# Kernel optimization log

Hardware: AMD Instinct MI355X
Metric: run time of the kernel (lower is better)

Reference implementation:

```python
import jax, jax.numpy as jnp
import numpy as np

EPS = 1e-6

def l2norm(x):
    return x / jnp.maximum(jnp.linalg.norm(x, axis=-1, keepdims=True), 1e-12)

def setup_inputs() -> dict:
    key = jax.random.key(0)
    ks = jax.random.split(key, 16)
    B, V, L = 64, 197, 64
    Dv, Dt, E = 768, 768, 256
    s = (2.0 / E) ** 0.5  # kaiming fan_out scale
    inp = {
        'visual_cls': jax.random.normal(ks[0], (B, Dv), jnp.float32),
        'textual_cls': jax.random.normal(ks[1], (B, Dt), jnp.float32),
        'visual_tokens': jax.random.normal(ks[2], (B, V, Dv), jnp.float32),
        'textual_tokens': jax.random.normal(ks[3], (B, L, Dt), jnp.float32),
        'text_length': jnp.maximum(jax.random.randint(ks[4], (B,), 0, L, jnp.int32), 1),
        'Wv': jax.random.normal(ks[5], (Dv, E), jnp.float32) * s,
        'bv': jnp.zeros((E,), jnp.float32),
        'Wt': jax.random.normal(ks[6], (Dt, E), jnp.float32) * s,
        'bt': jnp.zeros((E,), jnp.float32),
        'Wvt': jax.random.normal(ks[7], (Dv, E), jnp.float32) * s,
        'bvt': jnp.zeros((E,), jnp.float32),
        'Wtt': jax.random.normal(ks[8], (Dt, E), jnp.float32) * s,
        'btt': jnp.zeros((E,), jnp.float32),
    }
    return inp

def reference(visual_cls, textual_cls, visual_tokens, textual_tokens, text_length,
              Wv, bv, Wt, bt, Wvt, bvt, Wtt, btt):
    # cls projections
    v_cls = visual_cls @ Wv + bv            # [B, E]
    t_cls = textual_cls @ Wt + bt           # [B, E]
    # token projections + l2 normalize
    v_tok = l2norm(visual_tokens @ Wvt + bvt)   # [B, V, E]
    t_tok = l2norm(textual_tokens @ Wtt + btt)  # [B, L, E]
    B, V, E = v_tok.shape
    L = t_tok.shape[1]
    # full cross-modal token similarity (this is the kernel target)
    sim = jnp.einsum('bvd,qtd->bqvt', v_tok, t_tok)  # [B, Q, V, T]
    # image->text: max over text tokens, plain mean over visual tokens
    image_to_text = jnp.max(sim, axis=-1)            # [B, Q, V]
    image_to_text_sim = jnp.sum(image_to_text, axis=-1) / V  # [B, Q]
    # text->image: max over visual tokens, masked mean over text tokens
    text_to_image = jnp.max(sim, axis=-2)            # [B, Q, T]
    # faithful to original: mask indexed by FIRST batch axis b
    mask = jnp.arange(L)[None, :] >= text_length[:, None]   # [B, T]
    mask3 = mask[:, None, :]                                 # [B, 1, T]
    numer = jnp.sum(jnp.where(mask3, 0.0, text_to_image), axis=-1)
    denom = jnp.maximum(jnp.sum(~mask3, axis=-1).astype(text_to_image.dtype), EPS)
    text_to_image_sim = numer / denom                # [B, Q]
    return (v_cls, t_cls, image_to_text_sim, text_to_image_sim)
```

## Files before the change

### kernel.cpp

```cpp
#include <hip/hip_runtime.h>
#include <hip/hip_bf16.h>

#define NB 64
#define NV 197
#define NL 64
#define ND 768
#define NE 256

typedef __attribute__((ext_vector_type(8))) short bh8;
typedef __attribute__((ext_vector_type(16))) float f32x16;

__device__ inline ushort f2bf(float x) {
  __hip_bfloat16 h = __float2bfloat16(x);
  return *reinterpret_cast<ushort*>(&h);
}

__device__ inline bh8 cvt8(float4 a, float4 b) {
  union { bh8 v; ushort u[8]; } r;
  r.u[0] = f2bf(a.x); r.u[1] = f2bf(a.y); r.u[2] = f2bf(a.z); r.u[3] = f2bf(a.w);
  r.u[4] = f2bf(b.x); r.u[5] = f2bf(b.y); r.u[6] = f2bf(b.z); r.u[7] = f2bf(b.w);
  return r.v;
}

__global__ __launch_bounds__(256) void wcvt_kernel(
    const float* __restrict__ W0, const float* __restrict__ W1,
    const float* __restrict__ W2, const float* __restrict__ W3,
    ushort* __restrict__ O0, ushort* __restrict__ O1,
    ushort* __restrict__ O2, ushort* __restrict__ O3) {
  const float* Win; ushort* Wout;
  switch (blockIdx.y) {
    case 0: Win = W0; Wout = O0; break;
    case 1: Win = W1; Wout = O1; break;
    case 2: Win = W2; Wout = O2; break;
    default: Win = W3; Wout = O3; break;
  }
  const int ks = blockIdx.x;
  const int t = threadIdx.x;
  const int l = t & 63;
  const int lr = l & 31, hi = l >> 5;
  const int kbase = ks * 16 + hi * 8;
#pragma unroll
  for (int i = 0; i < 2; ++i) {
    const int nt = (t >> 6) + i * 4;
    const int n = nt * 32 + lr;
    union { bh8 v; ushort u[8]; } f;
#pragma unroll
    for (int e = 0; e < 8; ++e)
      f.u[e] = f2bf(Win[(size_t)(kbase + e) * NE + n]);
    *(bh8*)&Wout[(size_t)((nt * 48 + ks) * 64 + l) * 8] = f.v;
  }
}

__device__ inline int aswz(int row, int cbyte) {
  return ((row * 256 + cbyte) ^ ((row & 15) << 4)) >> 2;
}

__global__ __launch_bounds__(256, 2) void proj_kernel(
    const float* __restrict__ Xv, const float* __restrict__ Xt,
    const float* __restrict__ Xcv, const float* __restrict__ Xct,
    const ushort* __restrict__ Fv, const ushort* __restrict__ Ft,
    const ushort* __restrict__ Fcv, const ushort* __restrict__ Fct,
    const float* __restrict__ bvt, const float* __restrict__ btt,
    const float* __restrict__ bv, const float* __restrict__ bt,
    ushort* __restrict__ v_tok, ushort* __restrict__ t_tok,
    float* __restrict__ v_cls, float* __restrict__ t_cls) {
  __shared__ float a_lds[64 * 64];
  __shared__ float ssq_lds[2][2][32];

  const int blk = blockIdx.x;
  const float* X; const ushort* F; const float* bias;
  ushort* outb = nullptr; float* outf = nullptr;
  int row0; bool norm;
  if (blk < 197)       { X = Xv;  F = Fv;  bias = bvt; outb = v_tok; row0 = blk * 64;         norm = true; }
  else if (blk < 261)  { X = Xt;  F = Ft;  bias = btt; outb = t_tok; row0 = (blk - 197) * 64; norm = true; }
  else if (blk == 261) { X = Xcv; F = Fcv; bias = bv;  outf = v_cls; row0 = 0;                norm = false; }
  else                 { X = Xct; F = Fct; bias = bt;  outf = t_cls; row0 = 0;                norm = false; }

  const int t = threadIdx.x;
  const int l = t & 63, w = t >> 6;
  const int lr = l & 31, hi = l >> 5;
  const int wr = w & 1, wc = w >> 1;

  const int srow = t >> 2;
  const int scq = t & 3;
  const float* Xrow = X + (size_t)(row0 + srow) * ND;

  const int arow = wr * 32 + lr;
  const ushort* Fw = F + ((size_t)(wc * 4 * 48) * 64 + l) * 8;

  f32x16 acc0 = {0}, acc1 = {0}, acc2 = {0}, acc3 = {0};

  float4 g0, g1, g2, g3, n0, n1, n2, n3;
#define GLOAD(d0, d1, d2, d3, kc) \
  d0 = *(const float4*)(Xrow + (kc) + scq * 4); \
  d1 = *(const float4*)(Xrow + (kc) + 16 + scq * 4); \
  d2 = *(const float4*)(Xrow + (kc) + 32 + scq * 4); \
  d3 = *(const float4*)(Xrow + (kc) + 48 + scq * 4);

  GLOAD(g0, g1, g2, g3, 0)
  for (int c = 0; c < 12; ++c) {
    if (c) __syncthreads();
    *(float4*)&a_lds[aswz(srow, scq * 16)]       = g0;
    *(float4*)&a_lds[aswz(srow, 64 + scq * 16)]  = g1;
    *(float4*)&a_lds[aswz(srow, 128 + scq * 16)] = g2;
    *(float4*)&a_lds[aswz(srow, 192 + scq * 16)] = g3;
    if (c < 11) { GLOAD(n0, n1, n2, n3, (c + 1) * 64) }
    __syncthreads();

#pragma unroll
    for (int ksl = 0; ksl < 4; ++ksl) {
      const int ks = c * 4 + ksl;
      float4 af0 = *(const float4*)&a_lds[aswz(arow, ksl * 64 + hi * 32)];
      float4 af1 = *(const float4*)&a_lds[aswz(arow, ksl * 64 + hi * 32 + 16)];
      bh8 b0 = *(const bh8*)(Fw + (size_t)(0 * 48 + ks) * 64 * 8);
      bh8 b1 = *(const bh8*)(Fw + (size_t)(1 * 48 + ks) * 64 * 8);
      bh8 b2 = *(const bh8*)(Fw + (size_t)(2 * 48 + ks) * 64 * 8);
      bh8 b3 = *(const bh8*)(Fw + (size_t)(3 * 48 + ks) * 64 * 8);
      bh8 af = cvt8(af0, af1);
      acc0 = __builtin_amdgcn_mfma_f32_32x32x16_bf16(af, b0, acc0, 0, 0, 0);
      acc1 = __builtin_amdgcn_mfma_f32_32x32x16_bf16(af, b1, acc1, 0, 0, 0);
      acc2 = __builtin_amdgcn_mfma_f32_32x32x16_bf16(af, b2, acc2, 0, 0, 0);
      acc3 = __builtin_amdgcn_mfma_f32_32x32x16_bf16(af, b3, acc3, 0, 0, 0);
    }
    g0 = n0; g1 = n1; g2 = n2; g3 = n3;
  }
#undef GLOAD

  const float bn0 = bias[wc * 128 + lr];
  const float bn1 = bias[wc * 128 + 32 + lr];
  const float bn2 = bias[wc * 128 + 64 + lr];
  const float bn3 = bias[wc * 128 + 96 + lr];
#pragma unroll
  for (int r = 0; r < 16; ++r) {
    acc0[r] += bn0; acc1[r] += bn1; acc2[r] += bn2; acc3[r] += bn3;
  }

  if (norm) {
    float p[16];
#pragma unroll
    for (int r = 0; r < 16; ++r)
      p[r] = acc0[r] * acc0[r] + acc1[r] * acc1[r] +
             acc2[r] * acc2[r] + acc3[r] * acc3[r];
#pragma unroll
    for (int off = 1; off < 32; off <<= 1) {
#pragma unroll
      for (int r = 0; r < 16; ++r) p[r] += __shfl_xor(p[r], off);
    }
    if (lr == 0) {
#pragma unroll
      for (int r = 0; r < 16; ++r)
        ssq_lds[wc][wr][(r & 3) + 8 * (r >> 2) + 4 * hi] = p[r];
    }
    __syncthreads();
#pragma unroll
    for (int r = 0; r < 16; ++r) {
      const int R = (r & 3) + 8 * (r >> 2) + 4 * hi;
      const float s = ssq_lds[0][wr][R] + ssq_lds[1][wr][R];
      const float scale = 1.0f / fmaxf(sqrtf(s), 1e-12f);
      ushort* orow = outb + (size_t)(row0 + wr * 32 + R) * NE + wc * 128 + lr;
      orow[0]  = f2bf(acc0[r] * scale);
      orow[32] = f2bf(acc1[r] * scale);
      orow[64] = f2bf(acc2[r] * scale);
      orow[96] = f2bf(acc3[r] * scale);
    }
  } else {
#pragma unroll
    for (int r = 0; r < 16; ++r) {
      const int R = (r & 3) + 8 * (r >> 2) + 4 * hi;
      float* orow = outf + (size_t)(row0 + wr * 32 + R) * NE + wc * 128 + lr;
      orow[0]  = acc0[r];
      orow[32] = acc1[r];
      orow[64] = acc2[r];
      orow[96] = acc3[r];
    }
  }
}

__global__ __launch_bounds__(256, 2) void sim_kernel(
    const __hip_bfloat16* __restrict__ vt,
    const __hip_bfloat16* __restrict__ tt,
    const int* __restrict__ tlen,
    float* __restrict__ out_i2t,
    float* __restrict__ out_t2i) {
  __shared__ float red[4][4][64];
  __shared__ float wsum[4][4];

  const int blk = blockIdx.x;
  const int q = blk & 63;
  const int bc = blk >> 6;
  const int tid = threadIdx.x;
  const int l = tid & 63;
  const int w = tid >> 6;
  const int lr = l & 31;
  const int hi = l >> 5;
  const size_t bstride = (size_t)NV * NE;

  bh8 breg0[16], breg1[16];
  {
    const __hip_bfloat16* T0 = tt + ((size_t)(q * NL) + lr) * NE + hi * 8;
    const __hip_bfloat16* T1 = T0 + 32 * NE;
#pragma unroll
    for (int s = 0; s < 16; ++s) {
      breg0[s] = *(const bh8*)(T0 + s * 16);
      breg1[s] = *(const bh8*)(T1 + s * 16);
    }
  }

  const int r0 = 32 * w + lr;
  const int r1 = min(128 + 32 * w + lr, NV - 1);

  const __hip_bfloat16* A0 = vt + (size_t)(bc * 4) * bstride + (size_t)r0 * NE + hi * 8;
  const __hip_bfloat16* A1 = vt + (size_t)(bc * 4) * bstride + (size_t)r1 * NE + hi * 8;

  bh8 a0[4], a1[4];
#pragma unroll
  for (int s = 0; s < 4; ++s) {
    a0[s] = *(const bh8*)(A0 + s * 16);
    a1[s] = *(const bh8*)(A1 + s * 16);
  }

  for (int ib = 0; ib < 4; ++ib) {
    f32x16 acc00 = {0}, acc01 = {0}, acc10 = {0}, acc11 = {0};

    __builtin_amdgcn_s_setprio(1);
#pragma unroll
    for (int s = 0; s < 16; ++s) {
      bh8 va0 = a0[s & 3], va1 = a1[s & 3];
      const int sn = s + 4;
      const size_t off = (size_t)(sn & 15) * 16 + (size_t)(sn >> 4) * bstride;
      a0[s & 3] = *(const bh8*)(A0 + off);
      a1[s & 3] = *(const bh8*)(A1 + off);
      acc00 = __builtin_amdgcn_mfma_f32_32x32x16_bf16(va0, breg0[s], acc00, 0, 0, 0);
      acc01 = __builtin_amdgcn_mfma_f32_32x32x16_bf16(va0, breg1[s], acc01, 0, 0, 0);
      acc10 = __builtin_amdgcn_mfma_f32_32x32x16_bf16(va1, breg0[s], acc10, 0, 0, 0);
      acc11 = __builtin_amdgcn_mfma_f32_32x32x16_bf16(va1, breg1[s], acc11, 0, 0, 0);
    }
    __builtin_amdgcn_s_setprio(0);
    A0 += bstride;
    A1 += bstride;

    float i2t_sum = 0.0f;
#pragma unroll
    for (int r = 0; r < 16; ++r) {
      {
        float m = fmaxf(acc00[r], acc01[r]);
        m = fmaxf(m, __shfl_xor(m, 1));
        m = fmaxf(m, __shfl_xor(m, 2));
        m = fmaxf(m, __shfl_xor(m, 4));
        m = fmaxf(m, __shfl_xor(m, 8));
        m = fmaxf(m, __shfl_xor(m, 16));
        i2t_sum += m;
      }
      {
        float m = fmaxf(acc10[r], acc11[r]);
        m = fmaxf(m, __shfl_xor(m, 1));
        m = fmaxf(m, __shfl_xor(m, 2));
        m = fmaxf(m, __shfl_xor(m, 4));
        m = fmaxf(m, __shfl_xor(m, 8));
        m = fmaxf(m, __shfl_xor(m, 16));
        const int row = 128 + 32 * w + (r & 3) + 8 * (r >> 2) + 4 * hi;
        if (row < NV) i2t_sum += m;
      }
    }
    i2t_sum += __shfl_xor(i2t_sum, 32);
    if (l == 0) wsum[ib][w] = i2t_sum;

    float vm0 = -1e30f, vm1 = -1e30f;
#pragma unroll
    for (int r = 0; r < 16; ++r) {
      vm0 = fmaxf(vm0, fmaxf(acc00[r], acc10[r]));
      vm1 = fmaxf(vm1, fmaxf(acc01[r], acc11[r]));
    }
    vm0 = fmaxf(vm0, __shfl_xor(vm0, 32));
    vm1 = fmaxf(vm1, __shfl_xor(vm1, 32));
    if (hi == 0) red[ib][w][lr] = vm0;
    else         red[ib][w][32 + lr] = vm1;
  }

  __syncthreads();

  {
    const int ib = w;
    const int b = bc * 4 + ib;
    const int len = tlen[b];
    float m = fmaxf(fmaxf(red[ib][0][l], red[ib][1][l]),
                    fmaxf(red[ib][2][l], red[ib][3][l]));
    float v = (l < len) ? m : 0.0f;
#pragma unroll
    for (int off = 1; off < 64; off <<= 1) v += __shfl_xor(v, off);
    if (l == 0) {
      out_t2i[b * NB + q] = v / fmaxf((float)len, 1e-6f);
      out_i2t[b * NB + q] = (wsum[ib][0] + wsum[ib][1] +
                             wsum[ib][2] + wsum[ib][3]) / (float)NV;
    }
  }
}

extern "C" void kernel_launch(void* const* d_in, const int* in_sizes, int n_in,
                              void* d_out, int out_size, void* d_ws, size_t ws_size,
                              hipStream_t stream) {
  (void)in_sizes; (void)n_in; (void)out_size; (void)ws_size;
  const float* visual_cls    = (const float*)d_in[0];
  const float* textual_cls   = (const float*)d_in[1];
  const float* visual_tokens = (const float*)d_in[2];
  const float* textual_tokens= (const float*)d_in[3];
  const int*   text_length   = (const int*)d_in[4];
  const float* Wv  = (const float*)d_in[5];
  const float* bv  = (const float*)d_in[6];
  const float* Wt  = (const float*)d_in[7];
  const float* bt  = (const float*)d_in[8];
  const float* Wvt = (const float*)d_in[9];
  const float* bvt = (const float*)d_in[10];
  const float* Wtt = (const float*)d_in[11];
  const float* btt = (const float*)d_in[12];

  float* out   = (float*)d_out;
  float* v_cls = out;
  float* t_cls = out + NB * NE;
  float* i2t   = out + 2 * NB * NE;
  float* t2i   = i2t + NB * NB;

  ushort* wsb   = (ushort*)d_ws;
  ushort* v_tok = wsb;
  ushort* t_tok = v_tok + (size_t)NB * NV * NE;
  ushort* Fv    = t_tok + (size_t)NB * NL * NE;
  ushort* Ft    = Fv + (size_t)8 * 48 * 64 * 8;
  ushort* Fcv   = Ft + (size_t)8 * 48 * 64 * 8;
  ushort* Fct   = Fcv + (size_t)8 * 48 * 64 * 8;

  wcvt_kernel<<<dim3(48, 4), 256, 0, stream>>>(Wvt, Wtt, Wv, Wt,
                                               Fv, Ft, Fcv, Fct);
  proj_kernel<<<263, 256, 0, stream>>>(visual_tokens, textual_tokens,
                                       visual_cls, textual_cls,
                                       Fv, Ft, Fcv, Fct,
                                       bvt, btt, bv, bt,
                                       v_tok, t_tok, v_cls, t_cls);
  sim_kernel<<<NB * NB / 4, 256, 0, stream>>>((const __hip_bfloat16*)v_tok,
                                              (const __hip_bfloat16*)t_tok,
                                              text_length, i2t, t2i);
}
```

Measured before the change: 234.2 us.

## Store text tokens in MFMA fragment layout and stage them through LDS in sim kernel

The projection kernel now writes normalized text tokens directly in the MFMA operand fragment order, so the similarity kernel can bulk-copy one query's 64x256 text block into LDS instead of holding 32 fragments in registers. Each wave now handles one batch image and walks all visual-token tiles, keeping running column maxima in registers rather than reducing through shared memory across four batches per wave. Occupancy hint rises to 3 blocks per SM because register pressure drops. The cost is an extra 32 KB LDS fill per block and per-k LDS reads that replace register-resident operands.

```diff
diff --git a/kernel.cpp b/kernel.cpp
--- a/kernel.cpp
+++ b/kernel.cpp
@@ -51,10 +51,6 @@
   }
 }
 
-__device__ inline int aswz(int row, int cbyte) {
-  return ((row * 256 + cbyte) ^ ((row & 15) << 4)) >> 2;
-}
-
 __global__ __launch_bounds__(256, 2) void proj_kernel(
     const float* __restrict__ Xv, const float* __restrict__ Xt,
     const float* __restrict__ Xcv, const float* __restrict__ Xct,
@@ -62,7 +58,7 @@
     const ushort* __restrict__ Fcv, const ushort* __restrict__ Fct,
     const float* __restrict__ bvt, const float* __restrict__ btt,
     const float* __restrict__ bv, const float* __restrict__ bt,
-    ushort* __restrict__ v_tok, ushort* __restrict__ t_tok,
+    ushort* __restrict__ v_tok, ushort* __restrict__ t_frag,
     float* __restrict__ v_cls, float* __restrict__ t_cls) {
   __shared__ float a_lds[64 * 64];
   __shared__ float ssq_lds[2][2][32];
@@ -70,11 +66,11 @@
   const int blk = blockIdx.x;
   const float* X; const ushort* F; const float* bias;
   ushort* outb = nullptr; float* outf = nullptr;
-  int row0; bool norm;
-  if (blk < 197)       { X = Xv;  F = Fv;  bias = bvt; outb = v_tok; row0 = blk * 64;         norm = true; }
-  else if (blk < 261)  { X = Xt;  F = Ft;  bias = btt; outb = t_tok; row0 = (blk - 197) * 64; norm = true; }
-  else if (blk == 261) { X = Xcv; F = Fcv; bias = bv;  outf = v_cls; row0 = 0;                norm = false; }
-  else                 { X = Xct; F = Fct; bias = bt;  outf = t_cls; row0 = 0;                norm = false; }
+  int row0; bool norm; bool tfrag = false;
+  if (blk < 197)       { X = Xv;  F = Fv;  bias = bvt; outb = v_tok;  row0 = blk * 64;         norm = true; }
+  else if (blk < 261)  { X = Xt;  F = Ft;  bias = btt; outb = t_frag; row0 = (blk - 197) * 64; norm = true; tfrag = true; }
+  else if (blk == 261) { X = Xcv; F = Fcv; bias = bv;  outf = v_cls;  row0 = 0;                norm = false; }
+  else                 { X = Xct; F = Fct; bias = bt;  outf = t_cls;  row0 = 0;                norm = false; }
 
   const int t = threadIdx.x;
   const int l = t & 63, w = t >> 6;
@@ -97,21 +93,23 @@
   d2 = *(const float4*)(Xrow + (kc) + 32 + scq * 4); \
   d3 = *(const float4*)(Xrow + (kc) + 48 + scq * 4);
 
+#define ASWZ(row, cbyte) ((((row) * 256 + (cbyte)) ^ (((row) & 15) << 4)) >> 2)
+
   GLOAD(g0, g1, g2, g3, 0)
   for (int c = 0; c < 12; ++c) {
     if (c) __syncthreads();
-    *(float4*)&a_lds[aswz(srow, scq * 16)]       = g0;
-    *(float4*)&a_lds[aswz(srow, 64 + scq * 16)]  = g1;
-    *(float4*)&a_lds[aswz(srow, 128 + scq * 16)] = g2;
-    *(float4*)&a_lds[aswz(srow, 192 + scq * 16)] = g3;
+    *(float4*)&a_lds[ASWZ(srow, scq * 16)]       = g0;
+    *(float4*)&a_lds[ASWZ(srow, 64 + scq * 16)]  = g1;
+    *(float4*)&a_lds[ASWZ(srow, 128 + scq * 16)] = g2;
+    *(float4*)&a_lds[ASWZ(srow, 192 + scq * 16)] = g3;
     if (c < 11) { GLOAD(n0, n1, n2, n3, (c + 1) * 64) }
     __syncthreads();
 
 #pragma unroll
     for (int ksl = 0; ksl < 4; ++ksl) {
       const int ks = c * 4 + ksl;
-      float4 af0 = *(const float4*)&a_lds[aswz(arow, ksl * 64 + hi * 32)];
-      float4 af1 = *(const float4*)&a_lds[aswz(arow, ksl * 64 + hi * 32 + 16)];
+      float4 af0 = *(const float4*)&a_lds[ASWZ(arow, ksl * 64 + hi * 32)];
+      float4 af1 = *(const float4*)&a_lds[ASWZ(arow, ksl * 64 + hi * 32 + 16)];
       bh8 b0 = *(const bh8*)(Fw + (size_t)(0 * 48 + ks) * 64 * 8);
       bh8 b1 = *(const bh8*)(Fw + (size_t)(1 * 48 + ks) * 64 * 8);
       bh8 b2 = *(const bh8*)(Fw + (size_t)(2 * 48 + ks) * 64 * 8);
@@ -125,6 +123,7 @@
     g0 = n0; g1 = n1; g2 = n2; g3 = n3;
   }
 #undef GLOAD
+#undef ASWZ
 
   const float bn0 = bias[wc * 128 + lr];
   const float bn1 = bias[wc * 128 + 32 + lr];
@@ -152,16 +151,34 @@
         ssq_lds[wc][wr][(r & 3) + 8 * (r >> 2) + 4 * hi] = p[r];
     }
     __syncthreads();
-#pragma unroll
-    for (int r = 0; r < 16; ++r) {
-      const int R = (r & 3) + 8 * (r >> 2) + 4 * hi;
-      const float s = ssq_lds[0][wr][R] + ssq_lds[1][wr][R];
-      const float scale = 1.0f / fmaxf(sqrtf(s), 1e-12f);
-      ushort* orow = outb + (size_t)(row0 + wr * 32 + R) * NE + wc * 128 + lr;
-      orow[0]  = f2bf(acc0[r] * scale);
-      orow[32] = f2bf(acc1[r] * scale);
-      orow[64] = f2bf(acc2[r] * scale);
-      orow[96] = f2bf(acc3[r] * scale);
+    if (!tfrag) {
+#pragma unroll
+      for (int r = 0; r < 16; ++r) {
+        const int R = (r & 3) + 8 * (r >> 2) + 4 * hi;
+        const float s = ssq_lds[0][wr][R] + ssq_lds[1][wr][R];
+        const float scale = 1.0f / fmaxf(sqrtf(s), 1e-12f);
+        ushort* orow = outb + (size_t)(row0 + wr * 32 + R) * NE + wc * 128 + lr;
+        orow[0]  = f2bf(acc0[r] * scale);
+        orow[32] = f2bf(acc1[r] * scale);
+        orow[64] = f2bf(acc2[r] * scale);
+        orow[96] = f2bf(acc3[r] * scale);
+      }
+    } else {
+      ushort* tq = outb + (size_t)(row0 >> 6) * 16384;
+      const int cA = lr >> 4;
+      const int cB = ((lr >> 3) & 1) * 32;
+      const int cE = lr & 7;
+#pragma unroll
+      for (int r = 0; r < 16; ++r) {
+        const int R = (r & 3) + 8 * (r >> 2) + 4 * hi;
+        const float s = ssq_lds[0][wr][R] + ssq_lds[1][wr][R];
+        const float scale = 1.0f / fmaxf(sqrtf(s), 1e-12f);
+        const int base = ((wr * 16 + wc * 8 + cA) * 64 + R + cB) * 8 + cE;
+        tq[base]        = f2bf(acc0[r] * scale);
+        tq[base + 1024] = f2bf(acc1[r] * scale);
+        tq[base + 2048] = f2bf(acc2[r] * scale);
+        tq[base + 3072] = f2bf(acc3[r] * scale);
+      }
     }
   } else {
 #pragma unroll
@@ -176,123 +193,112 @@
   }
 }
 
-__global__ __launch_bounds__(256, 2) void sim_kernel(
-    const __hip_bfloat16* __restrict__ vt,
-    const __hip_bfloat16* __restrict__ tt,
+__global__ __launch_bounds__(256, 3) void sim_kernel(
+    const ushort* __restrict__ vt, const ushort* __restrict__ tfrag,
     const int* __restrict__ tlen,
-    float* __restrict__ out_i2t,
-    float* __restrict__ out_t2i) {
-  __shared__ float red[4][4][64];
-  __shared__ float wsum[4][4];
+    float* __restrict__ out_i2t, float* __restrict__ out_t2i) {
+  __shared__ ushort t_lds[16384];
 
   const int blk = blockIdx.x;
   const int q = blk & 63;
   const int bc = blk >> 6;
   const int tid = threadIdx.x;
-  const int l = tid & 63;
-  const int w = tid >> 6;
-  const int lr = l & 31;
-  const int hi = l >> 5;
-  const size_t bstride = (size_t)NV * NE;
-
-  bh8 breg0[16], breg1[16];
+
   {
-    const __hip_bfloat16* T0 = tt + ((size_t)(q * NL) + lr) * NE + hi * 8;
-    const __hip_bfloat16* T1 = T0 + 32 * NE;
-#pragma unroll
-    for (int s = 0; s < 16; ++s) {
-      breg0[s] = *(const bh8*)(T0 + s * 16);
-      breg1[s] = *(const bh8*)(T1 + s * 16);
-    }
-  }
-
-  const int r0 = 32 * w + lr;
-  const int r1 = min(128 + 32 * w + lr, NV - 1);
-
-  const __hip_bfloat16* A0 = vt + (size_t)(bc * 4) * bstride + (size_t)r0 * NE + hi * 8;
-  const __hip_bfloat16* A1 = vt + (size_t)(bc * 4) * bstride + (size_t)r1 * NE + hi * 8;
-
-  bh8 a0[4], a1[4];
+    const bh8* src = (const bh8*)(tfrag + (size_t)q * 16384);
+    bh8* dst = (bh8*)t_lds;
+#pragma unroll
+    for (int j = 0; j < 8; ++j) dst[tid + j * 256] = src[tid + j * 256];
+  }
+  __syncthreads();
+
+  const int l = tid & 63, w = tid >> 6;
+  const int lr = l & 31, hi = l >> 5;
+  const int b = bc * 4 + w;
+  const int len = tlen[b];
+  const ushort* Vb = vt + (size_t)b * NV * NE + hi * 8;
+
+  int offA[4], offB[4];
+#pragma unroll
+  for (int p = 0; p < 4; ++p) {
+    offA[p] = min(p * 64 + lr, NV - 1) * NE;
+    offB[p] = min(p * 64 + 32 + lr, NV - 1) * NE;
+  }
+
+  bh8 rA[4], rB[4];
 #pragma unroll
   for (int s = 0; s < 4; ++s) {
-    a0[s] = *(const bh8*)(A0 + s * 16);
-    a1[s] = *(const bh8*)(A1 + s * 16);
-  }
-
-  for (int ib = 0; ib < 4; ++ib) {
-    f32x16 acc00 = {0}, acc01 = {0}, acc10 = {0}, acc11 = {0};
-
+    rA[s] = *(const bh8*)(Vb + offA[0] + s * 16);
+    rB[s] = *(const bh8*)(Vb + offB[0] + s * 16);
+  }
+
+  f32x16 vmax0, vmax1;
+#pragma unroll
+  for (int r = 0; r < 16; ++r) { vmax0[r] = -1e30f; vmax1[r] = -1e30f; }
+  float i2t_sum = 0.0f;
+
+#pragma unroll
+  for (int p = 0; p < 4; ++p) {
+    f32x16 a00 = {0}, a01 = {0}, a10 = {0}, a11 = {0};
     __builtin_amdgcn_s_setprio(1);
 #pragma unroll
-    for (int s = 0; s < 16; ++s) {
-      bh8 va0 = a0[s & 3], va1 = a1[s & 3];
-      const int sn = s + 4;
-      const size_t off = (size_t)(sn & 15) * 16 + (size_t)(sn >> 4) * bstride;
-      a0[s & 3] = *(const bh8*)(A0 + off);
-      a1[s & 3] = *(const bh8*)(A1 + off);
-      acc00 = __builtin_amdgcn_mfma_f32_32x32x16_bf16(va0, breg0[s], acc00, 0, 0, 0);
-      acc01 = __builtin_amdgcn_mfma_f32_32x32x16_bf16(va0, breg1[s], acc01, 0, 0, 0);
-      acc10 = __builtin_amdgcn_mfma_f32_32x32x16_bf16(va1, breg0[s], acc10, 0, 0, 0);
-      acc11 = __builtin_amdgcn_mfma_f32_32x32x16_bf16(va1, breg1[s], acc11, 0, 0, 0);
+    for (int ks = 0; ks < 16; ++ks) {
+      bh8 ta0 = *(const bh8*)&t_lds[(size_t)(ks * 64 + l) * 8];
+      bh8 ta1 = *(const bh8*)&t_lds[(size_t)((16 + ks) * 64 + l) * 8];
+      bh8 vb0 = rA[ks & 3], vb1 = rB[ks & 3];
+      int sn = p * 16 + ks + 4; if (sn > 63) sn = 63;
+      const int p2 = sn >> 4, k2 = sn & 15;
+      rA[ks & 3] = *(const bh8*)(Vb + offA[p2] + k2 * 16);
+      rB[ks & 3] = *(const bh8*)(Vb + offB[p2] + k2 * 16);
+      a00 = __builtin_amdgcn_mfma_f32_32x32x16_bf16(ta0, vb0, a00, 0, 0, 0);
+      a01 = __builtin_amdgcn_mfma_f32_32x32x16_bf16(ta0, vb1, a01, 0, 0, 0);
+      a10 = __builtin_amdgcn_mfma_f32_32x32x16_bf16(ta1, vb0, a10, 0, 0, 0);
+      a11 = __builtin_amdgcn_mfma_f32_32x32x16_bf16(ta1, vb1, a11, 0, 0, 0);
     }
     __builtin_amdgcn_s_setprio(0);
-    A0 += bstride;
-    A1 += bstride;
-
-    float i2t_sum = 0.0f;
+
+    {
+      float m0 = fmaxf(a00[0], a10[0]);
+#pragma unroll
+      for (int r = 1; r < 16; ++r) m0 = fmaxf(m0, fmaxf(a00[r], a10[r]));
+      m0 = fmaxf(m0, __shfl_xor(m0, 32));
+      if ((p * 64 + lr) < NV && hi == 0) i2t_sum += m0;
+      float m1 = fmaxf(a01[0], a11[0]);
+#pragma unroll
+      for (int r = 1; r < 16; ++r) m1 = fmaxf(m1, fmaxf(a01[r], a11[r]));
+      m1 = fmaxf(m1, __shfl_xor(m1, 32));
+      if ((p * 64 + 32 + lr) < NV && hi == 0) i2t_sum += m1;
+    }
 #pragma unroll
     for (int r = 0; r < 16; ++r) {
-      {
-        float m = fmaxf(acc00[r], acc01[r]);
-        m = fmaxf(m, __shfl_xor(m, 1));
-        m = fmaxf(m, __shfl_xor(m, 2));
-        m = fmaxf(m, __shfl_xor(m, 4));
-        m = fmaxf(m, __shfl_xor(m, 8));
-        m = fmaxf(m, __shfl_xor(m, 16));
-        i2t_sum += m;
-      }
-      {
-        float m = fmaxf(acc10[r], acc11[r]);
-        m = fmaxf(m, __shfl_xor(m, 1));
-        m = fmaxf(m, __shfl_xor(m, 2));
-        m = fmaxf(m, __shfl_xor(m, 4));
-        m = fmaxf(m, __shfl_xor(m, 8));
-        m = fmaxf(m, __shfl_xor(m, 16));
-        const int row = 128 + 32 * w + (r & 3) + 8 * (r >> 2) + 4 * hi;
-        if (row < NV) i2t_sum += m;
-      }
-    }
-    i2t_sum += __shfl_xor(i2t_sum, 32);
-    if (l == 0) wsum[ib][w] = i2t_sum;
-
-    float vm0 = -1e30f, vm1 = -1e30f;
+      vmax0[r] = fmaxf(vmax0[r], fmaxf(a00[r], a01[r]));
+      vmax1[r] = fmaxf(vmax1[r], fmaxf(a10[r], a11[r]));
+    }
+  }
+
+#pragma unroll
+  for (int off = 1; off < 32; off <<= 1) {
 #pragma unroll
     for (int r = 0; r < 16; ++r) {
-      vm0 = fmaxf(vm0, fmaxf(acc00[r], acc10[r]));
-      vm1 = fmaxf(vm1, fmaxf(acc01[r], acc11[r]));
-    }
-    vm0 = fmaxf(vm0, __shfl_xor(vm0, 32));
-    vm1 = fmaxf(vm1, __shfl_xor(vm1, 32));
-    if (hi == 0) red[ib][w][lr] = vm0;
-    else         red[ib][w][32 + lr] = vm1;
-  }
-
-  __syncthreads();
-
-  {
-    const int ib = w;
-    const int b = bc * 4 + ib;
-    const int len = tlen[b];
-    float m = fmaxf(fmaxf(red[ib][0][l], red[ib][1][l]),
-                    fmaxf(red[ib][2][l], red[ib][3][l]));
-    float v = (l < len) ? m : 0.0f;
-#pragma unroll
-    for (int off = 1; off < 64; off <<= 1) v += __shfl_xor(v, off);
-    if (l == 0) {
-      out_t2i[b * NB + q] = v / fmaxf((float)len, 1e-6f);
-      out_i2t[b * NB + q] = (wsum[ib][0] + wsum[ib][1] +
-                             wsum[ib][2] + wsum[ib][3]) / (float)NV;
-    }
+      vmax0[r] = fmaxf(vmax0[r], __shfl_xor(vmax0[r], off));
+      vmax1[r] = fmaxf(vmax1[r], __shfl_xor(vmax1[r], off));
+    }
+  }
+  float tsum = 0.0f;
+#pragma unroll
+  for (int r = 0; r < 16; ++r) {
+    const int t0 = (r & 3) + 8 * (r >> 2) + 4 * hi;
+    if (t0 < len) tsum += vmax0[r];
+    if (32 + t0 < len) tsum += vmax1[r];
+  }
+  tsum += __shfl_xor(tsum, 32);
+
+#pragma unroll
+  for (int off = 1; off < 64; off <<= 1) i2t_sum += __shfl_xor(i2t_sum, off);
+
+  if (l == 0) {
+    out_t2i[b * NB + q] = tsum / fmaxf((float)len, 1e-6f);
+    out_i2t[b * NB + q] = i2t_sum / (float)NV;
   }
 }
 
@@ -320,13 +326,13 @@
   float* i2t   = out + 2 * NB * NE;
   float* t2i   = i2t + NB * NB;
 
-  ushort* wsb   = (ushort*)d_ws;
-  ushort* v_tok = wsb;
-  ushort* t_tok = v_tok + (size_t)NB * NV * NE;
-  ushort* Fv    = t_tok + (size_t)NB * NL * NE;
-  ushort* Ft    = Fv + (size_t)8 * 48 * 64 * 8;
-  ushort* Fcv   = Ft + (size_t)8 * 48 * 64 * 8;
-  ushort* Fct   = Fcv + (size_t)8 * 48 * 64 * 8;
+  ushort* wsb    = (ushort*)d_ws;
+  ushort* v_tok  = wsb;
+  ushort* t_frag = v_tok + (size_t)NB * NV * NE;
+  ushort* Fv     = t_frag + (size_t)NB * NL * NE;
+  ushort* Ft     = Fv + (size_t)8 * 48 * 64 * 8;
+  ushort* Fcv    = Ft + (size_t)8 * 48 * 64 * 8;
+  ushort* Fct    = Fcv + (size_t)8 * 48 * 64 * 8;
 
   wcvt_kernel<<<dim3(48, 4), 256, 0, stream>>>(Wvt, Wtt, Wv, Wt,
                                                Fv, Ft, Fcv, Fct);
@@ -334,8 +340,7 @@
                                        visual_cls, textual_cls,
                                        Fv, Ft, Fcv, Fct,
                                        bvt, btt, bv, bt,
-                                       v_tok, t_tok, v_cls, t_cls);
-  sim_kernel<<<NB * NB / 4, 256, 0, stream>>>((const __hip_bfloat16*)v_tok,
-                                              (const __hip_bfloat16*)t_tok,
+                                       v_tok, t_frag, v_cls, t_cls);
+  sim_kernel<<<NB * NB / 4, 256, 0, stream>>>(v_tok, t_frag,
                                               text_length, i2t, t2i);
 }
```

Result: slower. 480.4 us (+105.1%).
